# Optimization experiments

Measured on AMD Instinct MI355X. Metric: run time of the kernel, lower is better.

The kernel has to match this reference:

```python
import math
import jax, jax.numpy as jnp
import numpy as np

R, N, B, E, H, M = 128, 256, 1, 512, 8, 4
D = E // H
NEG = -1e9  # eye-mask fill value from masked_fill(-1000000000)


def setup_inputs() -> dict:
    key = jax.random.key(0)
    ks = jax.random.split(key, 10)
    p = lambda k, shape: jax.random.normal(k, shape, jnp.float32) * 0.02
    z = lambda n: jnp.zeros((n,), jnp.float32)
    return {
        "x": jax.random.normal(ks[0], (R, N, B, E), jnp.float32),
        "network": jax.random.uniform(ks[1], (B, N, N, M), jnp.float32),
        "Wq": p(ks[2], (E, E)), "bq": z(E),
        "Wk": p(ks[3], (E, E)), "bk": z(E),
        "Wv": p(ks[4], (E, E)), "bv": z(E),
        "Wo": p(ks[5], (E, E)), "bo": z(E),
        "Wq1": p(ks[6], (D, 8)), "bq1": z(8),
        "Wk1": p(ks[7], (1, 8)), "bk1": z(8),
        "l": jax.random.normal(ks[8], (H, 1, 1, 1), jnp.float32),
    }


def reference(x, network, Wq, bq, Wk, bk, Wv, bv, Wo, bo, Wq1, bq1, Wk1, bk1, l):
    # x: [R, N, B, E]; network: [B, N, N, M] (B must be 1, as in the torch module)
    scaling = (D ** -0.5) / math.sqrt(R)  # align_scaling

    q = (x @ Wq + bq).reshape(R, N, B, H, D) * scaling
    k = (x @ Wk + bk).reshape(R, N, B, H, D)

    # shared contraction: summed over rows r, kept per head-dim d -> [H, B, N, N, D]
    qk = jnp.einsum('rinhd,rjnhd->hnijd', q, k)

    # network-bias MLP branch
    q1 = (qk @ Wq1 + bq1).mean(0)                  # [B, N, N, 8]
    network_k = network[..., None] * Wk1[0] + bk1  # Linear(1,8): [B, N, N, M, 8]
    net_attn = jnp.einsum('nijd,nijmd->nijm', q1, network_k)  # [B, N, N, M]
    net_attn = jnp.tile(net_attn, (H, 1, 1, 1))    # repeat over heads (B==1) -> [H, N, N, M]

    # attn_weights 'rinhd,rjnhd->hnij' == qk summed over d
    attn_weights = qk.sum(-1)                      # [H, B, N, N]

    net_probs = jax.nn.softmax(net_attn, axis=-1)  # softmax over M network channels
    net_bias = (network * net_probs).sum(-1)[:, None, :, :]  # [H, 1(B), N, N]
    attn_weights = attn_weights + l * net_bias

    eye = jnp.eye(N, dtype=bool)
    attn_weights = jnp.where(eye, NEG, attn_weights)
    attn_probs = jax.nn.softmax(attn_weights, axis=-1)  # [H, B, N, N]

    v = (x @ Wv + bv).reshape(R, N, B, H, D)
    context = jnp.einsum('hnij,rjnhd->rinhd', attn_probs, v).reshape(R, N, B, E)
    output = context @ Wo + bo
    return (output, attn_probs, l)
```

## Files before the change

### kernel.cpp

```cpp
#include <hip/hip_runtime.h>
#include <hip/hip_bf16.h>
#include <cmath>
#include <stdint.h>

using bf16 = __hip_bfloat16;
typedef __attribute__((ext_vector_type(8))) short bf16x8;
typedef __attribute__((ext_vector_type(4))) float f32x4;

constexpr long HS = 2097152;

__device__ __forceinline__ void gload16(const bf16* g, bf16* l)
{
  __builtin_amdgcn_global_load_lds(
      (const __attribute__((address_space(1))) void*)g,
      (__attribute__((address_space(3))) void*)l,
      16, 0, 0);
}

__device__ __forceinline__ int swsrc(int c) { return (((c & 3) ^ ((c >> 3) & 3)) * 8); }

__global__ __launch_bounds__(256)
void k_convert_x(const float* __restrict__ x, bf16* __restrict__ xb)
{
  const long idx = (long)blockIdx.x * 256 + threadIdx.x;
  const float4 f0 = *(const float4*)&x[idx * 8];
  const float4 f1 = *(const float4*)&x[idx * 8 + 4];
  alignas(16) bf16 t[8] = {
    __float2bfloat16(f0.x), __float2bfloat16(f0.y),
    __float2bfloat16(f0.z), __float2bfloat16(f0.w),
    __float2bfloat16(f1.x), __float2bfloat16(f1.y),
    __float2bfloat16(f1.z), __float2bfloat16(f1.w)};
  *(uint4*)&xb[idx * 8] = *(const uint4*)t;
}

__global__ __launch_bounds__(256)
void k_prep_w(const float* __restrict__ Wq, const float* __restrict__ Wk,
              const float* __restrict__ Wv, const float* __restrict__ Wo,
              bf16* __restrict__ WT, float scaling)
{
  const int sel = blockIdx.z;
  const float* W = sel == 0 ? Wq : sel == 1 ? Wk : sel == 2 ? Wv : Wo;
  const float sc = sel == 0 ? scaling : 1.0f;
  const int k0 = blockIdx.x * 64, n0 = blockIdx.y * 64;
  __shared__ float tile[64][68];
  const int tid = threadIdx.x;
  #pragma unroll
  for (int it = 0; it < 4; it++) {
    const int c = tid + it * 256;
    const int kk = c >> 4, nn4 = (c & 15) * 4;
    const float4 v = *(const float4*)&W[(long)(k0 + kk) * 512 + n0 + nn4];
    tile[kk][nn4] = v.x; tile[kk][nn4 + 1] = v.y;
    tile[kk][nn4 + 2] = v.z; tile[kk][nn4 + 3] = v.w;
  }
  __syncthreads();
  #pragma unroll
  for (int it = 0; it < 2; it++) {
    const int c = tid + it * 256;
    const int nn = c >> 3, k8 = (c & 7) * 8;
    alignas(16) bf16 t[8];
    #pragma unroll
    for (int jj = 0; jj < 8; jj++) t[jj] = __float2bfloat16(tile[k8 + jj][nn] * sc);
    *(uint4*)&WT[(long)(sel * 512 + n0 + nn) * 512 + k0 + k8] = *(const uint4*)t;
  }
}

__global__ void k_prep_small(const float* __restrict__ bq, const float* __restrict__ bk,
                             const float* __restrict__ bv, const float* __restrict__ bo,
                             const float* __restrict__ Wq1, const float* __restrict__ Wk1,
                             float* __restrict__ bias_all, float* __restrict__ u, float scaling)
{
  const int idx = blockIdx.x * 256 + threadIdx.x;
  const int s2 = idx >> 9, n2 = idx & 511;
  const float* b = s2 == 0 ? bq : s2 == 1 ? bk : s2 == 2 ? bv : bo;
  bias_all[idx] = b[n2] * (s2 == 0 ? scaling : 1.0f);
  if (idx < 64) {
    float s = 0.0f;
    #pragma unroll
    for (int c = 0; c < 8; c++) s += Wq1[idx * 8 + c] * Wk1[c];
    u[idx] = s;
  }
}

__global__ __launch_bounds__(512, 2)
void gemm_qkv(const bf16* __restrict__ xb, const bf16* __restrict__ WT,
              const float* __restrict__ bias_all,
              bf16* __restrict__ Qn, bf16* __restrict__ Kn, bf16* __restrict__ Vj)
{
  __shared__ __align__(16) unsigned short smem[65536];
  bf16* As = (bf16*)smem;
  bf16* Bs = (bf16*)smem + 32768;
  const int tid = threadIdx.x, lane = tid & 63;
  const int wid = tid >> 6, wr = wid >> 2, wc = wid & 3;
  const int lr = lane & 15;
  const int lkx = ((lane >> 4) ^ ((lane >> 1) & 3)) * 8;
  const int flat = ((int)blockIdx.x & 7) * 96 + ((int)blockIdx.x >> 3);
  const int m0 = (flat / 6) * 256, nt = flat % 6, n0 = nt * 256;
  const int c1 = tid + 512;
  const int ra0 = tid >> 2, ra1 = c1 >> 2;
  const int ps0 = swsrc(tid), ps1 = swsrc(c1);
  f32x4 acc[8][4] = {};

  auto stage = [&](int b, int k0) {
    gload16(&xb[(long)(m0 + ra0) * 512 + k0 + ps0], &As[b * 8192 + tid * 8]);
    gload16(&xb[(long)(m0 + ra1) * 512 + k0 + ps1], &As[b * 8192 + c1 * 8]);
    gload16(&WT[(long)(n0 + ra0) * 512 + k0 + ps0], &Bs[b * 8192 + tid * 8]);
    gload16(&WT[(long)(n0 + ra1) * 512 + k0 + ps1], &Bs[b * 8192 + c1 * 8]);
  };

  stage(0, 0);
  stage(1, 32);
  stage(2, 64);

  for (int t = 0; t < 16; ++t) {
    const int cur = t & 3;
    if (t < 13) stage((t + 3) & 3, (t + 3) * 32);
    if (t == 0) {
      asm volatile("s_waitcnt vmcnt(12)" ::: "memory");
      __builtin_amdgcn_s_barrier();
    }
    bf16x8 af[8], bfr[4];
    #pragma unroll
    for (int n = 0; n < 4; n++)
      bfr[n] = *(const bf16x8*)&Bs[cur * 8192 + (wc * 64 + n * 16 + lr) * 32 + lkx];
    #pragma unroll
    for (int m = 0; m < 8; m++)
      af[m] = *(const bf16x8*)&As[cur * 8192 + (wr * 128 + m * 16 + lr) * 32 + lkx];
    __builtin_amdgcn_s_setprio(1);
    #pragma unroll
    for (int m = 0; m < 8; m++)
      #pragma unroll
      for (int n = 0; n < 4; n++)
        acc[m][n] = __builtin_amdgcn_mfma_f32_16x16x32_bf16(af[m], bfr[n], acc[m][n], 0, 0, 0);
    __builtin_amdgcn_s_setprio(0);
    if (t < 13)       asm volatile("s_waitcnt vmcnt(8)" ::: "memory");
    else if (t == 13) asm volatile("s_waitcnt vmcnt(4)" ::: "memory");
    else if (t == 14) asm volatile("s_waitcnt vmcnt(0)" ::: "memory");
    __builtin_amdgcn_s_barrier();
  }

  const int er = (lane >> 4) * 4, ec = lane & 15;
  if (nt < 4) {
    bf16* dst = (nt < 2) ? Qn : Kn;
    const int cb = (nt < 2) ? n0 : n0 - 512;
    #pragma unroll
    for (int m = 0; m < 8; m++) {
      const int row0 = m0 + wr * 128 + m * 16 + er;
      #pragma unroll
      for (int n = 0; n < 4; n++) {
        const int cw = wc * 64 + n * 16 + ec;
        const float bv = bias_all[n0 + cw];
        #pragma unroll
        for (int q = 0; q < 4; q++)
          dst[(long)(row0 + q) * 512 + cb + cw] = __float2bfloat16(acc[m][n][q] + bv);
      }
    }
  } else {
    bf16* vt = (bf16*)smem;
    const int r = m0 >> 8;
    const int hdbase = (nt - 4) * 256;
    #pragma unroll 1
    for (int p = 0; p < 4; ++p) {
      __syncthreads();
      if (wc == p) {
        #pragma unroll
        for (int m = 0; m < 8; m++) {
          const int rt0 = wr * 128 + m * 16 + er;
          #pragma unroll
          for (int n = 0; n < 4; n++) {
            const int ct = n * 16 + ec;
            const float bv = bias_all[n0 + p * 64 + ct];
            #pragma unroll
            for (int q = 0; q < 4; q++)
              vt[ct * 264 + rt0 + q] = __float2bfloat16(acc[m][n][q] + bv);
          }
        }
      }
      __syncthreads();
      #pragma unroll
      for (int cc = 0; cc < 4; cc++) {
        const int c = cc * 512 + tid;
        const int hl = c >> 5, tok8 = (c & 31) * 8;
        const uint4 v = *(const uint4*)&vt[hl * 264 + tok8];
        const int hd = hdbase + p * 64 + hl;
        const int h = hd >> 6, d = hd & 63;
        *(uint4*)&Vj[(long)h * HS + (long)(r * 64 + d) * 256 + tok8] = v;
      }
    }
  }
}

__global__ __launch_bounds__(256)
void gemm_logits(const bf16* __restrict__ Qn, const bf16* __restrict__ Kn,
                 const float* __restrict__ u, float* __restrict__ part)
{
  __shared__ bf16 As[4][128 * 32];
  __shared__ bf16 Bs[4][128 * 32];
  __shared__ float us[64];
  const int tid = threadIdx.x, lane = tid & 63;
  const int wid = tid >> 6, wr = wid >> 1, wc = wid & 1;
  const int lr = lane & 15;
  const int lkx = ((lane >> 4) ^ ((lane >> 1) & 3)) * 8;
  const int z = blockIdx.z, batch = z >> 2, ks = z & 3, h = batch & 7;
  const bool uscale = batch >= 8;
  const int m0 = blockIdx.y * 128, n0 = blockIdx.x * 128;
  if (tid < 64) us[tid] = u[tid];
  __syncthreads();
  const int c1 = tid + 256;
  const int ra0 = tid >> 2, ra1 = c1 >> 2;
  const int ps = swsrc(tid);
  f32x4 acc[4][4] = {};

  auto gk_of = [&](int kk) { return ks * 2048 + kk * 32; };

  if (!uscale) {
    auto stage = [&](int b, int kk) {
      const int gk = gk_of(kk), r = gk >> 6, d0 = gk & 63;
      const long ab = (long)(r * 256 + m0) * 512 + h * 64 + d0;
      const long bb = (long)(r * 256 + n0) * 512 + h * 64 + d0;
      gload16(&Qn[ab + (long)ra0 * 512 + ps], &As[b][tid * 8]);
      gload16(&Qn[ab + (long)ra1 * 512 + ps], &As[b][c1 * 8]);
      gload16(&Kn[bb + (long)ra0 * 512 + ps], &Bs[b][tid * 8]);
      gload16(&Kn[bb + (long)ra1 * 512 + ps], &Bs[b][c1 * 8]);
    };
    stage(0, 0);
    stage(1, 1);
    stage(2, 2);
    for (int kk = 0; kk < 64; ++kk) {
      const int cur = kk & 3;
      if (kk < 61) stage((kk + 3) & 3, kk + 3);
      if (kk == 0) {
        asm volatile("s_waitcnt vmcnt(12)" ::: "memory");
        __builtin_amdgcn_s_barrier();
      }
      bf16x8 af[4], bfr[4];
      #pragma unroll
      for (int m = 0; m < 4; m++)
        af[m] = *(const bf16x8*)&As[cur][(wr * 64 + m * 16 + lr) * 32 + lkx];
      #pragma unroll
      for (int n = 0; n < 4; n++)
        bfr[n] = *(const bf16x8*)&Bs[cur][(wc * 64 + n * 16 + lr) * 32 + lkx];
      __builtin_amdgcn_s_setprio(1);
      #pragma unroll
      for (int m = 0; m < 4; m++)
        #pragma unroll
        for (int n = 0; n < 4; n++)
          acc[m][n] = __builtin_amdgcn_mfma_f32_16x16x32_bf16(af[m], bfr[n], acc[m][n], 0, 0, 0);
      __builtin_amdgcn_s_setprio(0);
      if (kk < 61)       asm volatile("s_waitcnt vmcnt(8)" ::: "memory");
      else if (kk == 61) asm volatile("s_waitcnt vmcnt(4)" ::: "memory");
      else if (kk == 62) asm volatile("s_waitcnt vmcnt(0)" ::: "memory");
      __builtin_amdgcn_s_barrier();
    }
  } else {
    {
      const int gk = gk_of(0), r = gk >> 6, d0 = gk & 63;
      const long ab = (long)(r * 256 + m0) * 512 + h * 64 + d0;
      const long bb = (long)(r * 256 + n0) * 512 + h * 64 + d0;
      gload16(&Kn[bb + (long)ra0 * 512 + ps], &Bs[0][tid * 8]);
      gload16(&Kn[bb + (long)ra1 * 512 + ps], &Bs[0][c1 * 8]);
      const uint4 v0 = *(const uint4*)&Qn[ab + (long)ra0 * 512 + ps];
      const uint4 v1 = *(const uint4*)&Qn[ab + (long)ra1 * 512 + ps];
      const unsigned short* p0 = (const unsigned short*)&v0;
      const unsigned short* p1 = (const unsigned short*)&v1;
      alignas(16) bf16 t0[8], t1[8];
      #pragma unroll
      for (int jj = 0; jj < 8; jj++) {
        t0[jj] = __float2bfloat16(__bfloat162float(*(const bf16*)&p0[jj]) * us[d0 + ps + jj]);
        t1[jj] = __float2bfloat16(__bfloat162float(*(const bf16*)&p1[jj]) * us[d0 + ps + jj]);
      }
      *(uint4*)&As[0][tid * 8] = *(const uint4*)t0;
      *(uint4*)&As[0][c1 * 8] = *(const uint4*)t1;
    }
    __syncthreads();
    int buf = 0;
    for (int kk = 0; kk < 64; ++kk) {
      uint4 va0, va1;
      int d0n = 0;
      if (kk < 63) {
        const int gk = gk_of(kk + 1), r = gk >> 6;
        d0n = gk & 63;
        const long ab = (long)(r * 256 + m0) * 512 + h * 64 + d0n;
        const long bb = (long)(r * 256 + n0) * 512 + h * 64 + d0n;
        gload16(&Kn[bb + (long)ra0 * 512 + ps], &Bs[buf ^ 1][tid * 8]);
        gload16(&Kn[bb + (long)ra1 * 512 + ps], &Bs[buf ^ 1][c1 * 8]);
        va0 = *(const uint4*)&Qn[ab + (long)ra0 * 512 + ps];
        va1 = *(const uint4*)&Qn[ab + (long)ra1 * 512 + ps];
      }
      bf16x8 af[4], bfr[4];
      #pragma unroll
      for (int m = 0; m < 4; m++)
        af[m] = *(const bf16x8*)&As[buf][(wr * 64 + m * 16 + lr) * 32 + lkx];
      #pragma unroll
      for (int n = 0; n < 4; n++)
        bfr[n] = *(const bf16x8*)&Bs[buf][(wc * 64 + n * 16 + lr) * 32 + lkx];
      #pragma unroll
      for (int m = 0; m < 4; m++)
        #pragma unroll
        for (int n = 0; n < 4; n++)
          acc[m][n] = __builtin_amdgcn_mfma_f32_16x16x32_bf16(af[m], bfr[n], acc[m][n], 0, 0, 0);
      if (kk < 63) {
        const unsigned short* p0 = (const unsigned short*)&va0;
        const unsigned short* p1 = (const unsigned short*)&va1;
        alignas(16) bf16 t0[8], t1[8];
        #pragma unroll
        for (int jj = 0; jj < 8; jj++) {
          t0[jj] = __float2bfloat16(__bfloat162float(*(const bf16*)&p0[jj]) * us[d0n + ps + jj]);
          t1[jj] = __float2bfloat16(__bfloat162float(*(const bf16*)&p1[jj]) * us[d0n + ps + jj]);
        }
        *(uint4*)&As[buf ^ 1][tid * 8] = *(const uint4*)t0;
        *(uint4*)&As[buf ^ 1][c1 * 8] = *(const uint4*)t1;
      }
      __syncthreads();
      buf ^= 1;
    }
  }

  float* C = part + (long)z * 65536;
  const int er = (lane >> 4) * 4, ec = lane & 15;
  #pragma unroll
  for (int m = 0; m < 4; m++)
    #pragma unroll
    for (int n = 0; n < 4; n++) {
      const int col = n0 + wc * 64 + n * 16 + ec;
      #pragma unroll
      for (int q = 0; q < 4; q++)
        C[(long)(m0 + wr * 64 + m * 16 + er + q) * 256 + col] = acc[m][n][q];
    }
}

__global__ __launch_bounds__(256)
void gemm_ctx(const bf16* __restrict__ Pb, const bf16* __restrict__ Vj,
              bf16* __restrict__ ctxb)
{
  __shared__ bf16 As[3][128 * 32];
  __shared__ bf16 Bs[3][128 * 32];
  const int tid = threadIdx.x, lane = tid & 63;
  const int wid = tid >> 6, wr = wid >> 1, wc = wid & 1;
  const int lr = lane & 15;
  const int lkx = ((lane >> 4) ^ ((lane >> 1) & 3)) * 8;
  const int m0 = blockIdx.y * 128, n0 = blockIdx.x * 128, h = blockIdx.z;
  const bf16* A = Pb + (long)h * 65536;
  const bf16* B = Vj + (long)h * HS;
  const int c1 = tid + 256;
  const int ra0 = tid >> 2, ra1 = c1 >> 2;
  const int ps = swsrc(tid);
  f32x4 acc[4][4] = {};

  auto stage = [&](int b, int k0) {
    gload16(&A[(long)(m0 + ra0) * 256 + k0 + ps], &As[b][tid * 8]);
    gload16(&A[(long)(m0 + ra1) * 256 + k0 + ps], &As[b][c1 * 8]);
    gload16(&B[(long)(n0 + ra0) * 256 + k0 + ps], &Bs[b][tid * 8]);
    gload16(&B[(long)(n0 + ra1) * 256 + k0 + ps], &Bs[b][c1 * 8]);
  };

  stage(0, 0);
  stage(1, 32);

  for (int t = 0; t < 8; ++t) {
    const int cur = t % 3;
    if (t < 6) {
      stage((t + 2) % 3, (t + 2) * 32);
      asm volatile("s_waitcnt vmcnt(8)" ::: "memory");
    } else if (t == 6) {
      asm volatile("s_waitcnt vmcnt(4)" ::: "memory");
    } else {
      asm volatile("s_waitcnt vmcnt(0)" ::: "memory");
    }
    __builtin_amdgcn_s_barrier();
    bf16x8 af[4], bfr[4];
    #pragma unroll
    for (int m = 0; m < 4; m++)
      af[m] = *(const bf16x8*)&As[cur][(wr * 64 + m * 16 + lr) * 32 + lkx];
    #pragma unroll
    for (int n = 0; n < 4; n++)
      bfr[n] = *(const bf16x8*)&Bs[cur][(wc * 64 + n * 16 + lr) * 32 + lkx];
    #pragma unroll
    for (int m = 0; m < 4; m++)
      #pragma unroll
      for (int n = 0; n < 4; n++)
        acc[m][n] = __builtin_amdgcn_mfma_f32_16x16x32_bf16(af[m], bfr[n], acc[m][n], 0, 0, 0);
    __builtin_amdgcn_s_barrier();
  }

  const int er = (lane >> 4) * 4, ec = lane & 15;
  #pragma unroll
  for (int m = 0; m < 4; m++) {
    const int i0 = m0 + wr * 64 + m * 16 + er;
    #pragma unroll
    for (int n = 0; n < 4; n++) {
      const int col = n0 + wc * 64 + n * 16 + ec;
      const int rr = col >> 6, dd = col & 63;
      #pragma unroll
      for (int q = 0; q < 4; q++)
        ctxb[(long)(rr * 256 + i0 + q) * 512 + h * 64 + dd] = __float2bfloat16(acc[m][n][q]);
    }
  }
}

__global__ __launch_bounds__(512)
void gemm_outp(const bf16* __restrict__ A, const bf16* __restrict__ B,
               float* __restrict__ C, const float* __restrict__ bias)
{
  __shared__ bf16 As[3][128 * 32];
  __shared__ bf16 Bs[3][256 * 32];
  const int tid = threadIdx.x, lane = tid & 63, wid = tid >> 6;
  const int wr = wid >> 2, wc = wid & 3;
  const int lr = lane & 15;
  const int lkx = ((lane >> 4) ^ ((lane >> 1) & 3)) * 8;
  const int m0 = blockIdx.y * 128, n0 = blockIdx.x * 256;
  const int ra = tid >> 2;
  const int cb1 = tid + 512;
  const int rb0 = tid >> 2, rb1 = cb1 >> 2;
  const int ps = swsrc(tid);
  f32x4 acc[4][4] = {};

  auto stage = [&](int b, int k0) {
    gload16(&A[(long)(m0 + ra) * 512 + k0 + ps], &As[b][tid * 8]);
    gload16(&B[(long)(n0 + rb0) * 512 + k0 + ps], &Bs[b][tid * 8]);
    gload16(&B[(long)(n0 + rb1) * 512 + k0 + ps], &Bs[b][cb1 * 8]);
  };

  stage(0, 0);
  stage(1, 32);

  for (int t = 0; t < 16; ++t) {
    const int cur = t % 3;
    if (t < 14) {
      stage((t + 2) % 3, (t + 2) * 32);
      asm volatile("s_waitcnt vmcnt(6)" ::: "memory");
    } else if (t == 14) {
      asm volatile("s_waitcnt vmcnt(3)" ::: "memory");
    } else {
      asm volatile("s_waitcnt vmcnt(0)" ::: "memory");
    }
    __builtin_amdgcn_s_barrier();
    bf16x8 af[4], bfr[4];
    #pragma unroll
    for (int m = 0; m < 4; m++)
      af[m] = *(const bf16x8*)&As[cur][(wr * 64 + m * 16 + lr) * 32 + lkx];
    #pragma unroll
    for (int n = 0; n < 4; n++)
      bfr[n] = *(const bf16x8*)&Bs[cur][(wc * 64 + n * 16 + lr) * 32 + lkx];
    #pragma unroll
    for (int m = 0; m < 4; m++)
      #pragma unroll
      for (int n = 0; n < 4; n++)
        acc[m][n] = __builtin_amdgcn_mfma_f32_16x16x32_bf16(af[m], bfr[n], acc[m][n], 0, 0, 0);
    __builtin_amdgcn_s_barrier();
  }

  const int er = (lane >> 4) * 4, ec = lane & 15;
  #pragma unroll
  for (int m = 0; m < 4; m++) {
    const int row0 = m0 + wr * 64 + m * 16 + er;
    #pragma unroll
    for (int n = 0; n < 4; n++) {
      const int col = n0 + wc * 64 + n * 16 + ec;
      const float bv = bias[col];
      #pragma unroll
      for (int q = 0; q < 4; q++)
        C[(long)(row0 + q) * 512 + col] = acc[m][n][q] + bv;
    }
  }
}

__global__ void k_bias(const float* __restrict__ part, const float* __restrict__ network,
                       const float* __restrict__ bq1, const float* __restrict__ Wk1,
                       float* __restrict__ net_bias)
{
  const int i = blockIdx.x, j = threadIdx.x;
  float c1 = 0.0f;
  #pragma unroll
  for (int c = 0; c < 8; c++) c1 += bq1[c] * Wk1[c];
  float s1 = 0.0f;
  const long ij = i * 256 + j;
  #pragma unroll
  for (int s = 32; s < 64; s++) s1 += part[(long)s * 65536 + ij];
  s1 = 0.125f * s1 + c1;
  const float4 nw = *(const float4*)&network[ij * 4];
  const float a0 = nw.x * s1, a1 = nw.y * s1, a2 = nw.z * s1, a3 = nw.w * s1;
  const float mx = fmaxf(fmaxf(a0, a1), fmaxf(a2, a3));
  const float e0 = expf(a0 - mx), e1 = expf(a1 - mx), e2 = expf(a2 - mx), e3 = expf(a3 - mx);
  const float inv = 1.0f / (e0 + e1 + e2 + e3);
  net_bias[ij] = (nw.x * e0 + nw.y * e1 + nw.z * e2 + nw.w * e3) * inv;
}

__global__ void k_softmax(const float* __restrict__ part, const float* __restrict__ net_bias,
                          const float* __restrict__ l, float* __restrict__ out_probs,
                          bf16* __restrict__ Pb, float* __restrict__ out_l)
{
  const int i = blockIdx.x, h = blockIdx.y, j = threadIdx.x;
  const long ij = i * 256 + j;
  float w = 0.0f;
  #pragma unroll
  for (int ks = 0; ks < 4; ks++) w += part[(long)(h * 4 + ks) * 65536 + ij];
  w += l[h] * net_bias[ij];
  if (j == i) w = -1e9f;
  float m = w;
  #pragma unroll
  for (int o = 32; o; o >>= 1) m = fmaxf(m, __shfl_xor(m, o));
  __shared__ float red[4], red2[4];
  if ((j & 63) == 0) red[j >> 6] = m;
  __syncthreads();
  m = fmaxf(fmaxf(red[0], red[1]), fmaxf(red[2], red[3]));
  const float e = expf(w - m);
  float s = e;
  #pragma unroll
  for (int o = 32; o; o >>= 1) s += __shfl_xor(s, o);
  if ((j & 63) == 0) red2[j >> 6] = s;
  __syncthreads();
  s = red2[0] + red2[1] + red2[2] + red2[3];
  const float p = e / s;
  out_probs[(long)h * 65536 + ij] = p;
  Pb[(long)h * 65536 + ij] = __float2bfloat16(p);
  if (h == 0 && i == 0 && j < 8) out_l[j] = l[j];
}

extern "C" void kernel_launch(void* const* d_in, const int* in_sizes, int n_in,
                              void* d_out, int out_size, void* d_ws, size_t ws_size,
                              hipStream_t stream)
{
  const float* x   = (const float*)d_in[0];
  const float* net = (const float*)d_in[1];
  const float* Wq  = (const float*)d_in[2];
  const float* bq  = (const float*)d_in[3];
  const float* Wk  = (const float*)d_in[4];
  const float* bk  = (const float*)d_in[5];
  const float* Wv  = (const float*)d_in[6];
  const float* bv  = (const float*)d_in[7];
  const float* Wo  = (const float*)d_in[8];
  const float* bo  = (const float*)d_in[9];
  const float* Wq1 = (const float*)d_in[10];
  const float* bq1 = (const float*)d_in[11];
  const float* Wk1 = (const float*)d_in[12];
  const float* l   = (const float*)d_in[14];
  float* out = (float*)d_out;

  bf16* Qn = (bf16*)d_out;
  bf16* Kn = Qn + 16777216;

  char* ws = (char*)d_ws;
  size_t off = 0;
  auto alloc = [&](size_t bytes) { char* p = ws + off; off += (bytes + 255) & ~255ULL; return p; };
  bf16*  WT       = (bf16*)alloc(2048ULL * 512 * 2);
  float* bias_all = (float*)alloc(2048 * 4);
  float* u        = (float*)alloc(64 * 4);
  bf16*  xb       = (bf16*)alloc(16777216ULL * 2);
  bf16*  Vj       = (bf16*)alloc(16777216ULL * 2);
  float* net_bias = (float*)alloc(65536ULL * 4);
  bf16*  Pb       = (bf16*)alloc(8ULL * 65536 * 2);
  float* part     = (float*)xb;
  bf16*  ctxb     = xb;

  const float scaling = (float)(0.125 / sqrt(128.0));

  k_convert_x<<<8192, 256, 0, stream>>>(x, xb);
  k_prep_w<<<dim3(8, 8, 4), 256, 0, stream>>>(Wq, Wk, Wv, Wo, WT, scaling);
  k_prep_small<<<8, 256, 0, stream>>>(bq, bk, bv, bo, Wq1, Wk1, bias_all, u, scaling);

  gemm_qkv<<<768, 512, 0, stream>>>(xb, WT, bias_all, Qn, Kn, Vj);

  gemm_logits<<<dim3(2, 2, 64), 256, 0, stream>>>(Qn, Kn, u, part);

  k_bias<<<256, 256, 0, stream>>>(part, net, bq1, Wk1, net_bias);
  k_softmax<<<dim3(256, 8, 1), 256, 0, stream>>>(part, net_bias, l,
                                                 out + 16777216, Pb, out + 17301504);

  gemm_ctx<<<dim3(64, 2, 8), 256, 0, stream>>>(Pb, Vj, ctxb);

  gemm_outp<<<dim3(2, 256, 1), 512, 0, stream>>>(ctxb, WT + 1536 * 512, out, bias_all + 1536);
}
```

Measured before the change: 188.8 us.

## Fuse plain and u-scaled logit GEMMs sharing Q/K tile loads

The logits GEMM used to launch separate batches for the plain Q·K product and the u-scaled product, each loading the same Q and K tiles. Now each block loads the tiles once, scales the A fragments in registers by u, and issues two MFMA streams into two accumulators. The split-K factor goes from 4 to 8 so there are still enough blocks. In exchange it doubles accumulator register pressure, adds per-element scaling work in the inner loop, and doubles the partial-sum traffic that the bias and softmax kernels read.

New measurement: 192.7 us. +2.1%, slower.

```diff
diff --git a/kernel.cpp b/kernel.cpp
--- a/kernel.cpp
+++ b/kernel.cpp
@@ -200,122 +200,78 @@
   const int wid = tid >> 6, wr = wid >> 1, wc = wid & 1;
   const int lr = lane & 15;
   const int lkx = ((lane >> 4) ^ ((lane >> 1) & 3)) * 8;
-  const int z = blockIdx.z, batch = z >> 2, ks = z & 3, h = batch & 7;
-  const bool uscale = batch >= 8;
+  const int z = blockIdx.z, h = z >> 3, ks = z & 7;
   const int m0 = blockIdx.y * 128, n0 = blockIdx.x * 128;
   if (tid < 64) us[tid] = u[tid];
   __syncthreads();
+  float ufa[8], ufb[8];
+  #pragma unroll
+  for (int j = 0; j < 8; j++) { ufa[j] = us[lkx + j]; ufb[j] = us[32 + lkx + j]; }
   const int c1 = tid + 256;
   const int ra0 = tid >> 2, ra1 = c1 >> 2;
   const int ps = swsrc(tid);
-  f32x4 acc[4][4] = {};
-
-  auto gk_of = [&](int kk) { return ks * 2048 + kk * 32; };
-
-  if (!uscale) {
-    auto stage = [&](int b, int kk) {
-      const int gk = gk_of(kk), r = gk >> 6, d0 = gk & 63;
-      const long ab = (long)(r * 256 + m0) * 512 + h * 64 + d0;
-      const long bb = (long)(r * 256 + n0) * 512 + h * 64 + d0;
-      gload16(&Qn[ab + (long)ra0 * 512 + ps], &As[b][tid * 8]);
-      gload16(&Qn[ab + (long)ra1 * 512 + ps], &As[b][c1 * 8]);
-      gload16(&Kn[bb + (long)ra0 * 512 + ps], &Bs[b][tid * 8]);
-      gload16(&Kn[bb + (long)ra1 * 512 + ps], &Bs[b][c1 * 8]);
-    };
-    stage(0, 0);
-    stage(1, 1);
-    stage(2, 2);
-    for (int kk = 0; kk < 64; ++kk) {
-      const int cur = kk & 3;
-      if (kk < 61) stage((kk + 3) & 3, kk + 3);
-      if (kk == 0) {
-        asm volatile("s_waitcnt vmcnt(12)" ::: "memory");
-        __builtin_amdgcn_s_barrier();
+  f32x4 acc[4][4] = {}, accu[4][4] = {};
+
+  auto stage = [&](int b, int kk) {
+    const int gk = ks * 1024 + kk * 32;
+    const int r = gk >> 6, d0 = gk & 63;
+    const long ab = (long)(r * 256 + m0) * 512 + h * 64 + d0;
+    const long bb = (long)(r * 256 + n0) * 512 + h * 64 + d0;
+    gload16(&Qn[ab + (long)ra0 * 512 + ps], &As[b][tid * 8]);
+    gload16(&Qn[ab + (long)ra1 * 512 + ps], &As[b][c1 * 8]);
+    gload16(&Kn[bb + (long)ra0 * 512 + ps], &Bs[b][tid * 8]);
+    gload16(&Kn[bb + (long)ra1 * 512 + ps], &Bs[b][c1 * 8]);
+  };
+
+  stage(0, 0);
+  stage(1, 1);
+  stage(2, 2);
+
+  for (int kk = 0; kk < 32; ++kk) {
+    const int cur = kk & 3;
+    if (kk < 29) stage((kk + 3) & 3, kk + 3);
+    if (kk == 0) {
+      asm volatile("s_waitcnt vmcnt(12)" ::: "memory");
+      __builtin_amdgcn_s_barrier();
+    }
+    const bool odd = (kk & 1) != 0;
+    bf16x8 af[4], bfr[4], afu[4];
+    #pragma unroll
+    for (int m = 0; m < 4; m++)
+      af[m] = *(const bf16x8*)&As[cur][(wr * 64 + m * 16 + lr) * 32 + lkx];
+    #pragma unroll
+    for (int n = 0; n < 4; n++)
+      bfr[n] = *(const bf16x8*)&Bs[cur][(wc * 64 + n * 16 + lr) * 32 + lkx];
+    #pragma unroll
+    for (int m = 0; m < 4; m++) {
+      #pragma unroll
+      for (int j = 0; j < 8; j++) {
+        const unsigned short a_ = (unsigned short)af[m][j];
+        const float f = __bfloat162float(*(const bf16*)&a_) * (odd ? ufb[j] : ufa[j]);
+        const bf16 b_ = __float2bfloat16(f);
+        afu[m][j] = *(const short*)&b_;
       }
-      bf16x8 af[4], bfr[4];
-      #pragma unroll
-      for (int m = 0; m < 4; m++)
-        af[m] = *(const bf16x8*)&As[cur][(wr * 64 + m * 16 + lr) * 32 + lkx];
+    }
+    __builtin_amdgcn_s_setprio(1);
+    #pragma unroll
+    for (int m = 0; m < 4; m++)
       #pragma unroll
       for (int n = 0; n < 4; n++)
-        bfr[n] = *(const bf16x8*)&Bs[cur][(wc * 64 + n * 16 + lr) * 32 + lkx];
-      __builtin_amdgcn_s_setprio(1);
-      #pragma unroll
-      for (int m = 0; m < 4; m++)
-        #pragma unroll
-        for (int n = 0; n < 4; n++)
-          acc[m][n] = __builtin_amdgcn_mfma_f32_16x16x32_bf16(af[m], bfr[n], acc[m][n], 0, 0, 0);
-      __builtin_amdgcn_s_setprio(0);
-      if (kk < 61)       asm volatile("s_waitcnt vmcnt(8)" ::: "memory");
-      else if (kk == 61) asm volatile("s_waitcnt vmcnt(4)" ::: "memory");
-      else if (kk == 62) asm volatile("s_waitcnt vmcnt(0)" ::: "memory");
-      __builtin_amdgcn_s_barrier();
-    }
-  } else {
-    {
-      const int gk = gk_of(0), r = gk >> 6, d0 = gk & 63;
-      const long ab = (long)(r * 256 + m0) * 512 + h * 64 + d0;
-      const long bb = (long)(r * 256 + n0) * 512 + h * 64 + d0;
-      gload16(&Kn[bb + (long)ra0 * 512 + ps], &Bs[0][tid * 8]);
-      gload16(&Kn[bb + (long)ra1 * 512 + ps], &Bs[0][c1 * 8]);
-      const uint4 v0 = *(const uint4*)&Qn[ab + (long)ra0 * 512 + ps];
-      const uint4 v1 = *(const uint4*)&Qn[ab + (long)ra1 * 512 + ps];
-      const unsigned short* p0 = (const unsigned short*)&v0;
-      const unsigned short* p1 = (const unsigned short*)&v1;
-      alignas(16) bf16 t0[8], t1[8];
-      #pragma unroll
-      for (int jj = 0; jj < 8; jj++) {
-        t0[jj] = __float2bfloat16(__bfloat162float(*(const bf16*)&p0[jj]) * us[d0 + ps + jj]);
-        t1[jj] = __float2bfloat16(__bfloat162float(*(const bf16*)&p1[jj]) * us[d0 + ps + jj]);
-      }
-      *(uint4*)&As[0][tid * 8] = *(const uint4*)t0;
-      *(uint4*)&As[0][c1 * 8] = *(const uint4*)t1;
-    }
-    __syncthreads();
-    int buf = 0;
-    for (int kk = 0; kk < 64; ++kk) {
-      uint4 va0, va1;
-      int d0n = 0;
-      if (kk < 63) {
-        const int gk = gk_of(kk + 1), r = gk >> 6;
-        d0n = gk & 63;
-        const long ab = (long)(r * 256 + m0) * 512 + h * 64 + d0n;
-        const long bb = (long)(r * 256 + n0) * 512 + h * 64 + d0n;
-        gload16(&Kn[bb + (long)ra0 * 512 + ps], &Bs[buf ^ 1][tid * 8]);
-        gload16(&Kn[bb + (long)ra1 * 512 + ps], &Bs[buf ^ 1][c1 * 8]);
-        va0 = *(const uint4*)&Qn[ab + (long)ra0 * 512 + ps];
-        va1 = *(const uint4*)&Qn[ab + (long)ra1 * 512 + ps];
-      }
-      bf16x8 af[4], bfr[4];
-      #pragma unroll
-      for (int m = 0; m < 4; m++)
-        af[m] = *(const bf16x8*)&As[buf][(wr * 64 + m * 16 + lr) * 32 + lkx];
+        acc[m][n] = __builtin_amdgcn_mfma_f32_16x16x32_bf16(af[m], bfr[n], acc[m][n], 0, 0, 0);
+    #pragma unroll
+    for (int m = 0; m < 4; m++)
       #pragma unroll
       for (int n = 0; n < 4; n++)
-        bfr[n] = *(const bf16x8*)&Bs[buf][(wc * 64 + n * 16 + lr) * 32 + lkx];
-      #pragma unroll
-      for (int m = 0; m < 4; m++)
-        #pragma unroll
-        for (int n = 0; n < 4; n++)
-          acc[m][n] = __builtin_amdgcn_mfma_f32_16x16x32_bf16(af[m], bfr[n], acc[m][n], 0, 0, 0);
-      if (kk < 63) {
-        const unsigned short* p0 = (const unsigned short*)&va0;
-        const unsigned short* p1 = (const unsigned short*)&va1;
-        alignas(16) bf16 t0[8], t1[8];
-        #pragma unroll
-        for (int jj = 0; jj < 8; jj++) {
-          t0[jj] = __float2bfloat16(__bfloat162float(*(const bf16*)&p0[jj]) * us[d0n + ps + jj]);
-          t1[jj] = __float2bfloat16(__bfloat162float(*(const bf16*)&p1[jj]) * us[d0n + ps + jj]);
-        }
-        *(uint4*)&As[buf ^ 1][tid * 8] = *(const uint4*)t0;
-        *(uint4*)&As[buf ^ 1][c1 * 8] = *(const uint4*)t1;
-      }
-      __syncthreads();
-      buf ^= 1;
-    }
-  }
-
-  float* C = part + (long)z * 65536;
+        accu[m][n] = __builtin_amdgcn_mfma_f32_16x16x32_bf16(afu[m], bfr[n], accu[m][n], 0, 0, 0);
+    __builtin_amdgcn_s_setprio(0);
+    if (kk < 29)       asm volatile("s_waitcnt vmcnt(8)" ::: "memory");
+    else if (kk == 29) asm volatile("s_waitcnt vmcnt(4)" ::: "memory");
+    else if (kk == 30) asm volatile("s_waitcnt vmcnt(0)" ::: "memory");
+    __builtin_amdgcn_s_barrier();
+  }
+
+  float* C  = part + (long)z * 65536;
+  float* Cu = part + (long)(64 + z) * 65536;
   const int er = (lane >> 4) * 4, ec = lane & 15;
   #pragma unroll
   for (int m = 0; m < 4; m++)
@@ -323,8 +279,11 @@
     for (int n = 0; n < 4; n++) {
       const int col = n0 + wc * 64 + n * 16 + ec;
       #pragma unroll
-      for (int q = 0; q < 4; q++)
-        C[(long)(m0 + wr * 64 + m * 16 + er + q) * 256 + col] = acc[m][n][q];
+      for (int q = 0; q < 4; q++) {
+        const long idx = (long)(m0 + wr * 64 + m * 16 + er + q) * 256 + col;
+        C[idx]  = acc[m][n][q];
+        Cu[idx] = accu[m][n][q];
+      }
     }
 }
 
@@ -475,7 +434,7 @@
   float s1 = 0.0f;
   const long ij = i * 256 + j;
   #pragma unroll
-  for (int s = 32; s < 64; s++) s1 += part[(long)s * 65536 + ij];
+  for (int s = 64; s < 128; s++) s1 += part[(long)s * 65536 + ij];
   s1 = 0.125f * s1 + c1;
   const float4 nw = *(const float4*)&network[ij * 4];
   const float a0 = nw.x * s1, a1 = nw.y * s1, a2 = nw.z * s1, a3 = nw.w * s1;
@@ -493,7 +452,7 @@
   const long ij = i * 256 + j;
   float w = 0.0f;
   #pragma unroll
-  for (int ks = 0; ks < 4; ks++) w += part[(long)(h * 4 + ks) * 65536 + ij];
+  for (int ks = 0; ks < 8; ks++) w += part[(long)(h * 8 + ks) * 65536 + ij];
   w += l[h] * net_bias[ij];
   if (j == i) w = -1e9f;
   float m = w;
```
